# Performance work log

Measured on AMD Instinct MI355X. Metric: run time of the kernel, lower is better.

Reference implementation:

```python
import jax, jax.numpy as jnp
import numpy as np

N = 4096
FIN = 4096
LOC = 16
H1, H2, HEADS = 120, 50, 4
H1_PER = H1 // HEADS
FILM_Z = 32
SSDB_H = 60
N_HEMI = N // 2
NEG_SLOPE = 0.1
GATE_BIAS = -2.0
MASK_FILL = -9e15


def leaky(x):
    return jax.nn.leaky_relu(x, negative_slope=NEG_SLOPE)


def gat(x, mask, W, a_src, a_dst, bias, concat):
    # x: (N, Fin), W: (H, Fin, O), a_src/a_dst: (H, O), mask: (N, N) bool
    wh = jnp.einsum('nf,hfo->hno', x, W)            # (H, N, O)
    f1 = jnp.einsum('hno,ho->hn', wh, a_src)        # (H, N)
    f2 = jnp.einsum('hno,ho->hn', wh, a_dst)        # (H, N)
    e = leaky(f1[:, :, None] + f2[:, None, :])      # (H, N, N)
    e = jnp.where(mask[None], e, MASK_FILL)
    alpha = jax.nn.softmax(e, axis=-1)
    out = jnp.einsum('hij,hjo->hio', alpha, wh)     # (H, N, O)
    if concat:
        h, n, o = out.shape
        out2 = out.transpose(1, 0, 2).reshape(n, h * o)
    else:
        out2 = out.mean(axis=0)
    return out2 + bias


def _uni(k, shape, stdv):
    return jax.random.uniform(k, shape, jnp.float32, -stdv, stdv)


def setup_inputs() -> dict:
    key = jax.random.key(0)
    ks = jax.random.split(key, 30)
    s1 = 1.0 / np.sqrt(H1_PER)
    s2 = 1.0 / np.sqrt(H2)
    inp = {
        'x_fc': jax.random.normal(ks[0], (N, FIN), jnp.float32),
        'adj': jax.random.randint(ks[1], (N, N), 0, 2, jnp.int32),
        'l_loc': jax.random.uniform(ks[2], (N, LOC), jnp.float32),
        # gat1
        'W1': _uni(ks[3], (HEADS, FIN, H1_PER), s1),
        'a1s': _uni(ks[4], (HEADS, H1_PER), s1),
        'a1d': _uni(ks[5], (HEADS, H1_PER), s1),
        'b1': _uni(ks[6], (H1,), s1),
        # gat2
        'W2': _uni(ks[7], (1, H1, H2), s2),
        'a2s': _uni(ks[8], (1, H2), s2),
        'a2d': _uni(ks[9], (1, H2), s2),
        'b2': _uni(ks[10], (H2,), s2),
        # classifier (no bias)
        'Wc': _uni(ks[11], (2, H2), s2),
        # FiLM trunk
        'Wl1': _uni(ks[12], (FILM_Z, LOC), 1.0 / np.sqrt(LOC)),
        'bl1': _uni(ks[13], (FILM_Z,), 1.0 / np.sqrt(LOC)),
        'Wl2': _uni(ks[14], (FILM_Z, FILM_Z), 1.0 / np.sqrt(FILM_Z)),
        'bl2': _uni(ks[15], (FILM_Z,), 1.0 / np.sqrt(FILM_Z)),
        'Wg': _uni(ks[16], (H2, FILM_Z), 1.0 / np.sqrt(FILM_Z)),
        'bg': _uni(ks[17], (H2,), 1.0 / np.sqrt(FILM_Z)),
        'Wb': _uni(ks[18], (H2, FILM_Z), 1.0 / np.sqrt(FILM_Z)),
        'bb': _uni(ks[19], (H2,), 1.0 / np.sqrt(FILM_Z)),
        'Wgate': _uni(ks[20], (1, FILM_Z), 1.0 / np.sqrt(FILM_Z)),
        'bgate': jnp.full((1,), GATE_BIAS, jnp.float32),
        # SSDB hemi
        'Ws1': _uni(ks[21], (SSDB_H, N_HEMI), 1.0 / np.sqrt(N_HEMI)),
        'bs1': _uni(ks[22], (SSDB_H,), 1.0 / np.sqrt(N_HEMI)),
        'Ws2': _uni(ks[23], (1, SSDB_H), 1.0 / np.sqrt(SSDB_H)),
        'bs2': _uni(ks[24], (1,), 1.0 / np.sqrt(SSDB_H)),
    }
    return inp


def reference(x_fc, adj, l_loc, W1, a1s, a1d, b1, W2, a2s, a2d, b2, Wc,
              Wl1, bl1, Wl2, bl2, Wg, bg, Wb, bb, Wgate, bgate,
              Ws1, bs1, Ws2, bs2):
    mask = adj > 0
    h = leaky(gat(x_fc, mask, W1, a1s, a1d, b1, concat=True))    # (N, 120)
    h = leaky(gat(h, mask, W2, a2s, a2d, b2, concat=False))      # (N, 50)
    # FiLM conditioning
    z = leaky(l_loc @ Wl1.T + bl1)
    z = leaky(z @ Wl2.T + bl2)
    gamma = z @ Wg.T + bg                                        # (N, 50)
    beta = z @ Wb.T + bb                                         # (N, 50)
    g = jax.nn.sigmoid(z @ Wgate.T + bgate)                      # (N, 1)
    cov = jnp.clip(l_loc[:, -1], 0.0, 1.0)                       # coverage_power = 1.0
    g = g * cov[:, None]
    h_fused = h + g * (gamma * h + beta)
    logits = leaky(h_fused @ Wc.T)                               # (N, 2)
    # hemisphere SSDB bias
    t = logits.T                                                 # (2, N)
    ipsi = t[:, :N_HEMI]
    contra = t[:, N_HEMI:2 * N_HEMI]
    h_i = leaky(ipsi @ Ws1.T + bs1)                              # (2, 60)
    h_c = leaky(contra @ Ws1.T + bs1)
    b_i = leaky(h_i @ Ws2.T + bs2)                               # (2, 1)
    b_c = leaky(h_c @ Ws2.T + bs2)
    b_mid = 0.5 * (b_i + b_c)                                    # (2, 1)
    bias_nodes = jnp.concatenate([
        jnp.broadcast_to(b_i.T, (N_HEMI, 2)),
        jnp.broadcast_to(b_c.T, (N_HEMI, 2)),
    ], axis=0)                                                   # n_mid = 0
    logits = logits + bias_nodes
    bias_avg = b_mid[:, 0]                                       # (2,)
    return logits, bias_avg
```

## Files before the change

kernel.cpp:

```cpp
#include <hip/hip_runtime.h>

#define NN 4096
#define NNP 4128
#define BROW 132
#define HEADS 4
#define H1PER 30
#define H1DIM 120
#define H2DIM 50

typedef short short8_t __attribute__((ext_vector_type(8)));
typedef float f32x4 __attribute__((ext_vector_type(4)));

__device__ __forceinline__ float lrelu(float x) { return x > 0.f ? x : 0.1f * x; }

__device__ __forceinline__ unsigned short bfrne(float x) {
  unsigned u = __float_as_uint(x);
  u += 0x7fffu + ((u >> 16) & 1u);
  return (unsigned short)(u >> 16);
}
__device__ __forceinline__ unsigned bfpk_rne(float lo, float hi) {
  return (unsigned)bfrne(lo) | ((unsigned)bfrne(hi) << 16);
}
__device__ __forceinline__ unsigned bfpk(float lo, float hi) {
  unsigned a = (__float_as_uint(lo) + 0x8000u) >> 16;
  unsigned b = (__float_as_uint(hi) + 0x8000u) & 0xffff0000u;
  return a | b;
}
__device__ __forceinline__ unsigned fenc(float x) {
  unsigned u = __float_as_uint(x);
  return (u & 0x80000000u) ? ~u : (u | 0x80000000u);
}
__device__ __forceinline__ float fdec(unsigned u) {
  return (u & 0x80000000u) ? __uint_as_float(u ^ 0x80000000u) : __uint_as_float(~u);
}

__global__ __launch_bounds__(256) void k_bits(const int* __restrict__ adj,
                                              unsigned long long* __restrict__ bits) {
  int n = blockIdx.x >> 2, r = blockIdx.x & 3;
  size_t base = (size_t)n * 4096 + r * 1024;
  int t = threadIdx.x;
  int v0 = adj[base + t];
  int v1 = adj[base + 256 + t];
  int v2 = adj[base + 512 + t];
  int v3 = adj[base + 768 + t];
  unsigned long long m0 = __ballot(v0 > 0);
  unsigned long long m1 = __ballot(v1 > 0);
  unsigned long long m2 = __ballot(v2 > 0);
  unsigned long long m3 = __ballot(v3 > 0);
  if ((t & 63) == 0) {
    size_t w = (size_t)n * (BROW / 2) + r * 16 + (t >> 6);
    bits[w] = m0;
    bits[w + 4] = m1;
    bits[w + 8] = m2;
    bits[w + 12] = m3;
  }
}

__global__ __launch_bounds__(256) void k_prep(const float* __restrict__ W1,
                                              const float* __restrict__ a1s,
                                              const float* __restrict__ a1d,
                                              unsigned short* __restrict__ w1t) {
  int k = blockIdx.x * 256 + threadIdx.x;
#pragma unroll
  for (int h = 0; h < 4; ++h) {
    const float* wp = W1 + ((size_t)h * 4096 + k) * H1PER;
    float fs = 0.f, fd = 0.f;
#pragma unroll
    for (int oo = 0; oo < H1PER; ++oo) {
      float v = wp[oo];
      w1t[(size_t)(h * 30 + oo) * NNP + k] = bfrne(v);
      fs += v * a1s[h * H1PER + oo];
      fd += v * a1d[h * H1PER + oo];
    }
    w1t[(size_t)(120 + h) * NNP + k] = bfrne(fs);
    w1t[(size_t)(124 + h) * NNP + k] = bfrne(fd);
  }
}

__global__ __launch_bounds__(256) void k_gemm1s(const float* __restrict__ x,
                                                const unsigned short* __restrict__ w1t,
                                                float* __restrict__ part) {
  const int t = threadIdx.x;
  const int lane = t & 63, wave = t >> 6;
  const int m = lane & 15, q = lane >> 4;
  const int i0 = blockIdx.x * 32;
  const int kz = blockIdx.y * 512;
  const int r0 = (wave & 1) * 16;
  const int ntg0 = (wave >> 1) * 4;
  const float* xr = x + (size_t)(i0 + r0 + m) * 4096 + kz + q * 8;
  const unsigned short* wp = w1t + (size_t)m * NNP + kz + q * 8;
  f32x4 acc[4];
#pragma unroll
  for (int nt = 0; nt < 4; ++nt) acc[nt] = (f32x4){0.f, 0.f, 0.f, 0.f};
#pragma unroll
  for (int it = 0; it < 8; ++it) {
    const int kc = it * 64;
#pragma unroll
    for (int ks2 = 0; ks2 < 2; ++ks2) {
      const int ko = kc + ks2 * 32;
      float4 a0 = *(const float4*)(xr + ko);
      float4 a1 = *(const float4*)(xr + ko + 4);
      union { short8_t v; unsigned u[4]; } A;
      A.u[0] = bfpk_rne(a0.x, a0.y);
      A.u[1] = bfpk_rne(a0.z, a0.w);
      A.u[2] = bfpk_rne(a1.x, a1.y);
      A.u[3] = bfpk_rne(a1.z, a1.w);
      const unsigned short* wpp = wp + ko;
#pragma unroll
      for (int nt = 0; nt < 4; ++nt) {
        short8_t B = *(const short8_t*)(wpp + (size_t)(ntg0 + nt) * 16 * NNP);
        acc[nt] = __builtin_amdgcn_mfma_f32_16x16x32_bf16(A.v, B, acc[nt], 0, 0, 0);
      }
    }
  }
  float* pp = part + ((size_t)blockIdx.y * 4096 + i0 + r0 + q * 4) * 128 + ntg0 * 16 + m;
#pragma unroll
  for (int nt = 0; nt < 4; ++nt)
#pragma unroll
    for (int r = 0; r < 4; ++r) pp[r * 128 + nt * 16] = acc[nt][r];
}

__global__ __launch_bounds__(256) void k_f1c(const float* __restrict__ part,
                                             unsigned short* __restrict__ whbt,
                                             float* __restrict__ f1, float* __restrict__ f2,
                                             unsigned* __restrict__ mxu1) {
  const int t = threadIdx.x;
  const int n = blockIdx.x * 16 + (t >> 4);
  const int og = (t & 15) * 8;
  __shared__ float f2loc[16][4];
  float s[8] = {0.f, 0.f, 0.f, 0.f, 0.f, 0.f, 0.f, 0.f};
  for (int z = 0; z < 8; ++z) {
    const float* pp = part + ((size_t)z * NN + n) * 128 + og;
    float4 u0 = *(const float4*)pp;
    float4 u1 = *(const float4*)(pp + 4);
    s[0] += u0.x; s[1] += u0.y; s[2] += u0.z; s[3] += u0.w;
    s[4] += u1.x; s[5] += u1.y; s[6] += u1.z; s[7] += u1.w;
  }
  if (og < 120) {
#pragma unroll
    for (int j = 0; j < 8; ++j) {
      int o = og + j;
      int h = o / 30, oo = o - h * 30;
      whbt[(size_t)(h * 32 + oo) * NNP + n] = bfrne(s[j]);
    }
  } else {
#pragma unroll
    for (int j = 0; j < 4; ++j) {
      f1[(size_t)j * NN + n] = s[j];
      f2[(size_t)j * NN + n] = s[4 + j];
      f2loc[t >> 4][j] = s[4 + j];
    }
  }
  if ((t & 15) < 8) {
    int h = (t & 15) >> 1, odd = (t & 15) & 1;
    whbt[(size_t)(h * 32 + 30 + odd) * NNP + n] = odd ? 0 : 0x3f80;
  }
  __syncthreads();
  if (t < 4) {
    float m = f2loc[0][t];
#pragma unroll
    for (int i = 1; i < 16; ++i) m = fmaxf(m, f2loc[i][t]);
    atomicMax(&mxu1[t], fenc(m));
  }
}

__global__ __launch_bounds__(256) void k_att1m(const unsigned short* __restrict__ whbt,
                                               const float* __restrict__ f1, const float* __restrict__ f2,
                                               const unsigned* __restrict__ mxu1,
                                               const unsigned int* __restrict__ bits32,
                                               float* __restrict__ part) {
  const int h = blockIdx.y, js = blockIdx.z;
  const int t = threadIdx.x;
  const int lane = t & 63, wave = t >> 6;
  const int m = lane & 15, q = lane >> 4;
  const int i0 = blockIdx.x * 64 + wave * 16;
  const int jbase = js * 1024;
  const float mxh = fdec(mxu1[h]);
  __shared__ float2 es[1024];
  for (int e = t; e < 1024; e += 256) {
    float fv = f2[h * NN + jbase + e] - mxh;
    es[e] = make_float2(__expf(fv), __expf(0.1f * fv));
  }
  __syncthreads();
  const float f1r = f1[h * NN + i0 + m];
  const float s = f1r + mxh;
  const float R = __expf(fminf(60.f, -0.9f * s));
  const uint4* brow4 = (const uint4*)(bits32 + (size_t)(i0 + m) * BROW + (jbase >> 5));
  const unsigned short* bb0 = whbt + (size_t)(h * 32 + m) * NNP + jbase + q * 8;
  const unsigned short* bb1 = bb0 + 16 * NNP;
  const float2* fp = es + q * 8;
  f32x4 acc0 = {0.f, 0.f, 0.f, 0.f}, acc1 = {0.f, 0.f, 0.f, 0.f};
  for (int s4 = 0; s4 < 8; ++s4) {
    uint4 bq = brow4[s4];
#pragma unroll
    for (int sub = 0; sub < 4; ++sub) {
      const int step = s4 * 4 + sub;
      const int jl = step * 32;
      unsigned bsel = (sub == 0 ? bq.x : sub == 1 ? bq.y : sub == 2 ? bq.z : bq.w) >> (q * 8);
      float4 e01 = *(const float4*)(fp + jl);
      float4 e23 = *(const float4*)(fp + jl + 2);
      float4 e45 = *(const float4*)(fp + jl + 4);
      float4 e67 = *(const float4*)(fp + jl + 6);
      auto sc = [&](float ep, float en, int jj) {
        float wv = fmaxf(ep, R * en);
        return ((bsel >> jj) & 1u) ? wv : 0.f;
      };
      union { short8_t v; unsigned u[4]; } A;
      A.u[0] = bfpk(sc(e01.x, e01.y, 0), sc(e01.z, e01.w, 1));
      A.u[1] = bfpk(sc(e23.x, e23.y, 2), sc(e23.z, e23.w, 3));
      A.u[2] = bfpk(sc(e45.x, e45.y, 4), sc(e45.z, e45.w, 5));
      A.u[3] = bfpk(sc(e67.x, e67.y, 6), sc(e67.z, e67.w, 7));
      short8_t b0 = *(const short8_t*)(bb0 + jl);
      short8_t b1 = *(const short8_t*)(bb1 + jl);
      acc0 = __builtin_amdgcn_mfma_f32_16x16x32_bf16(A.v, b0, acc0, 0, 0, 0);
      acc1 = __builtin_amdgcn_mfma_f32_16x16x32_bf16(A.v, b1, acc1, 0, 0, 0);
    }
  }
  float* pp = part + ((size_t)(js * 4 + h) * NN + i0 + q * 4) * 32 + m;
#pragma unroll
  for (int r = 0; r < 4; ++r) {
    pp[r * 32] = acc0[r];
    pp[r * 32 + 16] = acc1[r];
  }
}

__global__ __launch_bounds__(256) void k_fuseA(const float* __restrict__ part, const float* __restrict__ b1,
                                               const float* __restrict__ W2, const float* __restrict__ a2s,
                                               const float* __restrict__ a2d,
                                               unsigned short* __restrict__ whbt2,
                                               float* __restrict__ f1b, float* __restrict__ f2b,
                                               unsigned* __restrict__ mxu2) {
  const int t = threadIdx.x;
  __shared__ float W2s[H1DIM * H2DIM];
  __shared__ float h1s[4][124];
  __shared__ float f2red[4];
  for (int e = t; e < H1DIM * H2DIM; e += 256) W2s[e] = W2[e];
  const int wv = t >> 6, lane = t & 63;
  const int n = blockIdx.x * 4 + wv;
  const int h = lane >> 4, o2 = (lane & 15) * 2;
  float tot0 = 0.f, tot1 = 0.f;
#pragma unroll
  for (int z = 0; z < 4; ++z) {
    const float* pp = part + ((size_t)(z * 4 + h) * NN + n) * 32 + o2;
    float2 u = *(const float2*)pp;
    tot0 += u.x;
    tot1 += u.y;
  }
  float l = __shfl(tot0, h * 16 + 15);
  float inv = 1.f / l;
  if (o2 < 30) {
    h1s[wv][h * 30 + o2] = lrelu(tot0 * inv + b1[h * 30 + o2]);
    h1s[wv][h * 30 + o2 + 1] = lrelu(tot1 * inv + b1[h * 30 + o2 + 1]);
  }
  __syncthreads();
  const int o = lane;
  float acc = 0.f;
  if (o < H2DIM) {
    const float* hr = h1s[wv];
#pragma unroll 4
    for (int k = 0; k < H1DIM; ++k) acc += hr[k] * W2s[k * H2DIM + o];
  }
  unsigned short wbv = (o < H2DIM) ? bfrne(acc) : (o == H2DIM ? (unsigned short)0x3f80 : (unsigned short)0);
  whbt2[(size_t)o * NNP + n] = wbv;
  float ps = (o < H2DIM) ? acc * a2s[o] : 0.f;
  float pd = (o < H2DIM) ? acc * a2d[o] : 0.f;
  for (int off = 32; off > 0; off >>= 1) {
    ps += __shfl_down(ps, off);
    pd += __shfl_down(pd, off);
  }
  if (lane == 0) {
    f1b[n] = ps;
    f2b[n] = pd;
    f2red[wv] = pd;
  }
  __syncthreads();
  if (t == 0) {
    float m = fmaxf(fmaxf(f2red[0], f2red[1]), fmaxf(f2red[2], f2red[3]));
    atomicMax(mxu2, fenc(m));
  }
}

__global__ __launch_bounds__(256) void k_att2m(const unsigned short* __restrict__ whbt2,
                                               const float* __restrict__ f1b, const float* __restrict__ f2b,
                                               const unsigned* __restrict__ mxu2,
                                               const unsigned int* __restrict__ bits32,
                                               float* __restrict__ part) {
  const int js = blockIdx.y;
  const int t = threadIdx.x;
  const int lane = t & 63, wave = t >> 6;
  const int m = lane & 15, q = lane >> 4;
  const int i0 = blockIdx.x * 64 + wave * 16;
  const int jbase = js * 512;
  const float mx0 = fdec(mxu2[0]);
  __shared__ float2 es[512];
  for (int e = t; e < 512; e += 256) {
    float fv = f2b[jbase + e] - mx0;
    es[e] = make_float2(__expf(fv), __expf(0.1f * fv));
  }
  __syncthreads();
  const float f1r = f1b[i0 + m];
  const float s = f1r + mx0;
  const float R = __expf(fminf(60.f, -0.9f * s));
  const uint4* brow4 = (const uint4*)(bits32 + (size_t)(i0 + m) * BROW + (jbase >> 5));
  const unsigned short* bb = whbt2 + (size_t)m * NNP + jbase + q * 8;
  const float2* fp = es + q * 8;
  f32x4 acc[4];
#pragma unroll
  for (int x = 0; x < 4; ++x) acc[x] = (f32x4){0.f, 0.f, 0.f, 0.f};
  for (int s4 = 0; s4 < 4; ++s4) {
    uint4 bq = brow4[s4];
#pragma unroll
    for (int sub = 0; sub < 4; ++sub) {
      const int step = s4 * 4 + sub;
      const int jl = step * 32;
      unsigned bsel = (sub == 0 ? bq.x : sub == 1 ? bq.y : sub == 2 ? bq.z : bq.w) >> (q * 8);
      float4 e01 = *(const float4*)(fp + jl);
      float4 e23 = *(const float4*)(fp + jl + 2);
      float4 e45 = *(const float4*)(fp + jl + 4);
      float4 e67 = *(const float4*)(fp + jl + 6);
      auto sc = [&](float ep, float en, int jj) {
        float wv = fmaxf(ep, R * en);
        return ((bsel >> jj) & 1u) ? wv : 0.f;
      };
      union { short8_t v; unsigned u[4]; } A;
      A.u[0] = bfpk(sc(e01.x, e01.y, 0), sc(e01.z, e01.w, 1));
      A.u[1] = bfpk(sc(e23.x, e23.y, 2), sc(e23.z, e23.w, 3));
      A.u[2] = bfpk(sc(e45.x, e45.y, 4), sc(e45.z, e45.w, 5));
      A.u[3] = bfpk(sc(e67.x, e67.y, 6), sc(e67.z, e67.w, 7));
#pragma unroll
      for (int tile = 0; tile < 4; ++tile) {
        short8_t b = *(const short8_t*)(bb + (size_t)tile * 16 * NNP + jl);
        acc[tile] = __builtin_amdgcn_mfma_f32_16x16x32_bf16(A.v, b, acc[tile], 0, 0, 0);
      }
    }
  }
  float* pp = part + ((size_t)js * NN + i0 + q * 4) * 64 + m;
#pragma unroll
  for (int tile = 0; tile < 4; ++tile)
#pragma unroll
    for (int r = 0; r < 4; ++r) pp[r * 64 + tile * 16] = acc[tile][r];
}

__global__ __launch_bounds__(256) void k_fuseB(const float* __restrict__ part, const float* __restrict__ b2,
                                               const float* __restrict__ l_loc,
                                               const float* __restrict__ Wl1, const float* __restrict__ bl1,
                                               const float* __restrict__ Wl2, const float* __restrict__ bl2,
                                               const float* __restrict__ Wg, const float* __restrict__ bg,
                                               const float* __restrict__ Wb, const float* __restrict__ bb,
                                               const float* __restrict__ Wgate, const float* __restrict__ bgate,
                                               const float* __restrict__ Wc, float* __restrict__ logits) {
  const int t = threadIdx.x;
  const int wv = t >> 6, lane = t & 63;
  const int n = blockIdx.x * 4 + wv;
  const float* p = part + (size_t)n * 64 + lane;
  float tot = 0.f;
#pragma unroll
  for (int z = 0; z < 8; ++z) tot += p[(size_t)z * NN * 64];
  float l = __shfl(tot, 50);
  float hv = (lane < H2DIM) ? lrelu(tot / l + b2[lane]) : 0.f;
  int r32 = lane & 31;
  float locv = l_loc[n * 16 + (lane & 15)];
  float cov = __shfl(locv, 15);
  cov = fminf(fmaxf(cov, 0.f), 1.f);
  float a1v = bl1[r32];
#pragma unroll
  for (int j = 0; j < 16; ++j) a1v += Wl1[r32 * 16 + j] * __shfl(locv, j);
  float z1 = lrelu(a1v);
  float a2v = bl2[r32];
#pragma unroll
  for (int j = 0; j < 32; ++j) a2v += Wl2[r32 * 32 + j] * __shfl(z1, j);
  float z2 = lrelu(a2v);
  float gs = bgate[0];
  float gam, bet;
  {
    int o = lane < H2DIM ? lane : 0;
    gam = bg[o];
    bet = bb[o];
#pragma unroll
    for (int j = 0; j < 32; ++j) {
      float zj = __shfl(z2, j);
      gs += Wgate[j] * zj;
      gam += Wg[o * 32 + j] * zj;
      bet += Wb[o * 32 + j] * zj;
    }
  }
  float g = cov / (1.f + __expf(-gs));
  float hf = hv + g * (gam * hv + bet);
  int o = lane < H2DIM ? lane : 0;
  float p0 = lane < H2DIM ? hf * Wc[o] : 0.f;
  float p1 = lane < H2DIM ? hf * Wc[H2DIM + o] : 0.f;
  for (int off = 32; off > 0; off >>= 1) {
    p0 += __shfl_down(p0, off);
    p1 += __shfl_down(p1, off);
  }
  if (lane == 0) {
    logits[n * 2 + 0] = lrelu(p0);
    logits[n * 2 + 1] = lrelu(p1);
  }
}

__global__ __launch_bounds__(64) void k_ssdbA(const float* __restrict__ logits,
                                              const float* __restrict__ Ws1, const float* __restrict__ bs1,
                                              const float* __restrict__ Ws2, float* __restrict__ hsum) {
  const int k = blockIdx.x, combo = blockIdx.y;
  const int hemi = combo >> 1, c = combo & 1;
  const int lane = threadIdx.x;
  const float* wr = Ws1 + (size_t)k * 2048;
  const float* lc = logits + (size_t)hemi * 4096 + c;
  float acc = 0.f;
#pragma unroll 4
  for (int i = lane; i < 2048; i += 64) acc += wr[i] * lc[2 * i];
  for (int off = 32; off > 0; off >>= 1) acc += __shfl_down(acc, off);
  if (lane == 0) hsum[combo * 60 + k] = lrelu(acc + bs1[k]) * Ws2[k];
}

__global__ __launch_bounds__(256) void k_finB(const float* __restrict__ hsum,
                                              const float* __restrict__ bs2,
                                              const float* __restrict__ logits,
                                              float* __restrict__ out) {
  __shared__ float Bs[4];
  const int t = threadIdx.x;
  {
    int combo = t >> 6, k = t & 63;
    float v = (k < 60) ? hsum[combo * 60 + k] : 0.f;
    for (int off = 32; off > 0; off >>= 1) v += __shfl_down(v, off);
    if (k == 0) Bs[combo] = lrelu(v + bs2[0]);
  }
  __syncthreads();
  int id = blockIdx.x * 256 + t;
  if (id < 2 * NN) {
    int n = id >> 1, c = id & 1;
    out[id] = logits[id] + Bs[(n < 2048 ? 0 : 2) + c];
  } else if (id < 2 * NN + 2) {
    int c = id - 2 * NN;
    out[id] = 0.5f * (Bs[c] + Bs[2 + c]);
  }
}

#define OFF_BITS 0
#define OFF_W1T 540672
#define OFF_GP 804864
#define OFF_A1P 804864
#define OFF_A2P 804864
#define OFF_WH1BT 4999168
#define OFF_F1A 5263360
#define OFF_F2A 5279744
#define OFF_WH2BT 5296128
#define OFF_F12 5428224
#define OFF_F22 5432320
#define OFF_LOG 5436416
#define OFF_MX 5444608
#define OFF_HS 5444672

extern "C" void kernel_launch(void* const* d_in, const int* in_sizes, int n_in,
                              void* d_out, int out_size, void* d_ws, size_t ws_size,
                              hipStream_t stream) {
  const float* x_fc  = (const float*)d_in[0];
  const int*   adj   = (const int*)d_in[1];
  const float* l_loc = (const float*)d_in[2];
  const float* W1    = (const float*)d_in[3];
  const float* a1s   = (const float*)d_in[4];
  const float* a1d   = (const float*)d_in[5];
  const float* b1    = (const float*)d_in[6];
  const float* W2    = (const float*)d_in[7];
  const float* a2s   = (const float*)d_in[8];
  const float* a2d   = (const float*)d_in[9];
  const float* b2    = (const float*)d_in[10];
  const float* Wc    = (const float*)d_in[11];
  const float* Wl1   = (const float*)d_in[12];
  const float* bl1   = (const float*)d_in[13];
  const float* Wl2   = (const float*)d_in[14];
  const float* bl2   = (const float*)d_in[15];
  const float* Wg    = (const float*)d_in[16];
  const float* bg    = (const float*)d_in[17];
  const float* Wb    = (const float*)d_in[18];
  const float* bb    = (const float*)d_in[19];
  const float* Wgate = (const float*)d_in[20];
  const float* bgate = (const float*)d_in[21];
  const float* Ws1   = (const float*)d_in[22];
  const float* bs1   = (const float*)d_in[23];
  const float* Ws2   = (const float*)d_in[24];
  const float* bs2   = (const float*)d_in[25];
  float* out = (float*)d_out;
  float* w = (float*)d_ws;
  unsigned long long* bits = (unsigned long long*)(w + OFF_BITS);
  const unsigned int* bits32 = (const unsigned int*)bits;
  unsigned short* wh1bt = (unsigned short*)(w + OFF_WH1BT);
  unsigned short* wh2bt = (unsigned short*)(w + OFF_WH2BT);
  unsigned short* w1t = (unsigned short*)(w + OFF_W1T);
  unsigned* mxu = (unsigned*)(w + OFF_MX);

  hipMemsetAsync(mxu, 0, 8 * sizeof(unsigned), stream);
  k_bits<<<NN * NN / 1024, 256, 0, stream>>>(adj, bits);
  k_prep<<<16, 256, 0, stream>>>(W1, a1s, a1d, w1t);
  k_gemm1s<<<dim3(128, 8), 256, 0, stream>>>(x_fc, w1t, w + OFF_GP);
  k_f1c<<<256, 256, 0, stream>>>(w + OFF_GP, wh1bt, w + OFF_F1A, w + OFF_F2A, mxu);
  k_att1m<<<dim3(64, HEADS, 4), 256, 0, stream>>>(wh1bt, w + OFF_F1A, w + OFF_F2A,
                                                  mxu, bits32, w + OFF_A1P);
  k_fuseA<<<1024, 256, 0, stream>>>(w + OFF_A1P, b1, W2, a2s, a2d, wh2bt,
                                    w + OFF_F12, w + OFF_F22, mxu + 4);
  k_att2m<<<dim3(64, 8), 256, 0, stream>>>(wh2bt, w + OFF_F12, w + OFF_F22,
                                           mxu + 4, bits32, w + OFF_A2P);
  k_fuseB<<<1024, 256, 0, stream>>>(w + OFF_A2P, b2, l_loc, Wl1, bl1, Wl2, bl2,
                                    Wg, bg, Wb, bb, Wgate, bgate, Wc, w + OFF_LOG);
  k_ssdbA<<<dim3(60, 4), 64, 0, stream>>>(w + OFF_LOG, Ws1, bs1, Ws2, w + OFF_HS);
  k_finB<<<33, 256, 0, stream>>>(w + OFF_HS, bs2, w + OFF_LOG, out);
}
```

Baseline: 335.8 us.

## Stage gemm1 operands through LDS with async global_load_lds double buffering

The first GAT projection GEMM now loads its x and W1 tiles into per-wave LDS buffers using the direct global-to-LDS load instruction. The buffers are double-buffered so the next k-slice streams in while MFMAs run on the current one, with XOR swizzles to avoid bank conflicts. This targets exposed global-load latency in the unpipelined register-load loop. In exchange it uses 48KB of LDS per block, which may reduce occupancy, and it relies on hand-written vmcnt waits.

```diff
diff --git a/kernel.cpp b/kernel.cpp
--- a/kernel.cpp
+++ b/kernel.cpp
@@ -33,6 +33,10 @@
 __device__ __forceinline__ float fdec(unsigned u) {
   return (u & 0x80000000u) ? __uint_as_float(u ^ 0x80000000u) : __uint_as_float(~u);
 }
+
+#define GL16(g, l)                                                                        \
+  __builtin_amdgcn_global_load_lds((const __attribute__((address_space(1))) unsigned int*)(g), \
+                                   (__attribute__((address_space(3))) unsigned int*)(l), 16, 0, 0)
 
 __global__ __launch_bounds__(256) void k_bits(const int* __restrict__ adj,
                                               unsigned long long* __restrict__ bits) {
@@ -87,30 +91,53 @@
   const int kz = blockIdx.y * 512;
   const int r0 = (wave & 1) * 16;
   const int ntg0 = (wave >> 1) * 4;
-  const float* xr = x + (size_t)(i0 + r0 + m) * 4096 + kz + q * 8;
-  const unsigned short* wp = w1t + (size_t)m * NNP + kz + q * 8;
+  __shared__ __align__(16) unsigned char lds[4][2][6144];
+  unsigned char* my0 = &lds[wave][0][0];
+  unsigned char* my1 = &lds[wave][1][0];
+  const int arow = lane >> 3;
+  const int agc = (lane & 7) ^ (arow & 7);
+  const int bgc = (lane & 3) ^ ((lane >> 3) & 3);
+  const float* gxa0 = x + (size_t)(i0 + r0 + arow) * 4096 + kz + agc * 4;
+  const float* gxa1 = gxa0 + (size_t)8 * 4096;
+  const unsigned short* gwb = w1t + (size_t)(ntg0 * 16 + (lane >> 2)) * NNP + kz + bgc * 8;
+  const int as0 = ((2 * q) ^ (m & 7)) * 16;
+  const int as1 = ((2 * q + 1) ^ (m & 7)) * 16;
+  const int bso = m * 64 + (q ^ ((m >> 1) & 3)) * 16;
+  const int abase = m * 128;
   f32x4 acc[4];
 #pragma unroll
   for (int nt = 0; nt < 4; ++nt) acc[nt] = (f32x4){0.f, 0.f, 0.f, 0.f};
-#pragma unroll
-  for (int it = 0; it < 8; ++it) {
-    const int kc = it * 64;
-#pragma unroll
-    for (int ks2 = 0; ks2 < 2; ++ks2) {
-      const int ko = kc + ks2 * 32;
-      float4 a0 = *(const float4*)(xr + ko);
-      float4 a1 = *(const float4*)(xr + ko + 4);
-      union { short8_t v; unsigned u[4]; } A;
-      A.u[0] = bfpk_rne(a0.x, a0.y);
-      A.u[1] = bfpk_rne(a0.z, a0.w);
-      A.u[2] = bfpk_rne(a1.x, a1.y);
-      A.u[3] = bfpk_rne(a1.z, a1.w);
-      const unsigned short* wpp = wp + ko;
-#pragma unroll
-      for (int nt = 0; nt < 4; ++nt) {
-        short8_t B = *(const short8_t*)(wpp + (size_t)(ntg0 + nt) * 16 * NNP);
-        acc[nt] = __builtin_amdgcn_mfma_f32_16x16x32_bf16(A.v, B, acc[nt], 0, 0, 0);
-      }
+
+  auto STAGE = [&](unsigned char* d, int kk) {
+    GL16(gxa0 + kk, d + lane * 16);
+    GL16(gxa1 + kk, d + 1024 + lane * 16);
+#pragma unroll
+    for (int c = 0; c < 4; ++c)
+      GL16(gwb + (size_t)c * 16 * NNP + kk, d + 2048 + c * 1024 + lane * 16);
+  };
+
+  STAGE(my0, 0);
+#pragma unroll
+  for (int it = 0; it < 16; ++it) {
+    unsigned char* cur = (it & 1) ? my1 : my0;
+    if (it < 15) {
+      STAGE((it & 1) ? my0 : my1, (it + 1) * 32);
+      asm volatile("s_waitcnt vmcnt(6)" ::: "memory");
+    } else {
+      asm volatile("s_waitcnt vmcnt(0)" ::: "memory");
+    }
+    __builtin_amdgcn_sched_barrier(0);
+    float4 a0 = *(const float4*)(cur + abase + as0);
+    float4 a1 = *(const float4*)(cur + abase + as1);
+    union { short8_t v; unsigned u[4]; } A;
+    A.u[0] = bfpk_rne(a0.x, a0.y);
+    A.u[1] = bfpk_rne(a0.z, a0.w);
+    A.u[2] = bfpk_rne(a1.x, a1.y);
+    A.u[3] = bfpk_rne(a1.z, a1.w);
+#pragma unroll
+    for (int nt = 0; nt < 4; ++nt) {
+      short8_t B = *(const short8_t*)(cur + 2048 + nt * 1024 + bso);
+      acc[nt] = __builtin_amdgcn_mfma_f32_16x16x32_bf16(A.v, B, acc[nt], 0, 0, 0);
     }
   }
   float* pp = part + ((size_t)blockIdx.y * 4096 + i0 + r0 + q * 4) * 128 + ntg0 * 16 + m;
```

After: 333.0 us. No clear change (-0.8%).

## Stage GEMM1 tiles into LDS with async double-buffered loads and 16-way split-K

Applied to the files above, without the earlier changes.

The first-layer projection GEMM now copies x and weight tiles into shared memory with global_load_lds, double-buffered and XOR-swizzled, so loads for the next step overlap the MFMAs on the current one. Before, each wave read operands straight from global memory with no reuse. The K split doubles from 8 to 16, which gives more blocks, and the reduction kernel and workspace offsets grow to match. The cost is a larger partial-sum buffer to write and reduce, plus barriers on every iteration.

```diff
diff --git a/kernel.cpp b/kernel.cpp
--- a/kernel.cpp
+++ b/kernel.cpp
@@ -33,6 +33,10 @@
 __device__ __forceinline__ float fdec(unsigned u) {
   return (u & 0x80000000u) ? __uint_as_float(u ^ 0x80000000u) : __uint_as_float(~u);
 }
+
+#define GL16(g, l)                                                                        \
+  __builtin_amdgcn_global_load_lds((const __attribute__((address_space(1))) unsigned int*)(g), \
+                                   (__attribute__((address_space(3))) unsigned int*)(l), 16, 0, 0)
 
 __global__ __launch_bounds__(256) void k_bits(const int* __restrict__ adj,
                                               unsigned long long* __restrict__ bits) {
@@ -84,34 +88,63 @@
   const int lane = t & 63, wave = t >> 6;
   const int m = lane & 15, q = lane >> 4;
   const int i0 = blockIdx.x * 32;
-  const int kz = blockIdx.y * 512;
+  const int kz = blockIdx.y * 256;
+  __shared__ float xs[2][32 * 32];
+  __shared__ unsigned short bsm[2][128 * 32];
   const int r0 = (wave & 1) * 16;
   const int ntg0 = (wave >> 1) * 4;
-  const float* xr = x + (size_t)(i0 + r0 + m) * 4096 + kz + q * 8;
-  const unsigned short* wp = w1t + (size_t)m * NNP + kz + q * 8;
+  const int ar = t >> 3;
+  const float* gxa = x + (size_t)(i0 + ar) * 4096 + kz + ((t & 7) ^ (ar & 7)) * 4;
+  const int adst = ar * 32 + (t & 7) * 4;
+  const int rB0 = t >> 2;
+  const int rB1 = 64 + (t >> 2);
+  const int gc0 = (t & 3) ^ (rB0 & 3) ^ ((rB0 >> 2) & 3);
+  const int gc1 = (t & 3) ^ (rB1 & 3) ^ ((rB1 >> 2) & 3);
+  const unsigned short* gwb0 = w1t + (size_t)rB0 * NNP + kz + gc0 * 8;
+  const unsigned short* gwb1 = w1t + (size_t)rB1 * NNP + kz + gc1 * 8;
+  const int bdst0 = rB0 * 32 + (t & 3) * 8;
+  const int bdst1 = rB1 * 32 + (t & 3) * 8;
+  const int arow = r0 + m;
+  const int as0 = ((2 * q) ^ (arow & 7)) * 4;
+  const int as1 = (((2 * q) + 1) ^ (arow & 7)) * 4;
   f32x4 acc[4];
 #pragma unroll
   for (int nt = 0; nt < 4; ++nt) acc[nt] = (f32x4){0.f, 0.f, 0.f, 0.f};
+
+  auto STAGE = [&](int buf, int kk) {
+    GL16(gxa + kk, &xs[buf][adst]);
+    GL16(gwb0 + kk, &bsm[buf][bdst0]);
+    GL16(gwb1 + kk, &bsm[buf][bdst1]);
+  };
+
+  STAGE(0, 0);
 #pragma unroll
   for (int it = 0; it < 8; ++it) {
-    const int kc = it * 64;
-#pragma unroll
-    for (int ks2 = 0; ks2 < 2; ++ks2) {
-      const int ko = kc + ks2 * 32;
-      float4 a0 = *(const float4*)(xr + ko);
-      float4 a1 = *(const float4*)(xr + ko + 4);
-      union { short8_t v; unsigned u[4]; } A;
-      A.u[0] = bfpk_rne(a0.x, a0.y);
-      A.u[1] = bfpk_rne(a0.z, a0.w);
-      A.u[2] = bfpk_rne(a1.x, a1.y);
-      A.u[3] = bfpk_rne(a1.z, a1.w);
-      const unsigned short* wpp = wp + ko;
-#pragma unroll
-      for (int nt = 0; nt < 4; ++nt) {
-        short8_t B = *(const short8_t*)(wpp + (size_t)(ntg0 + nt) * 16 * NNP);
-        acc[nt] = __builtin_amdgcn_mfma_f32_16x16x32_bf16(A.v, B, acc[nt], 0, 0, 0);
-      }
-    }
+    const int cur = it & 1;
+    if (it < 7) {
+      STAGE(cur ^ 1, (it + 1) * 32);
+      asm volatile("s_waitcnt vmcnt(3)" ::: "memory");
+    } else {
+      asm volatile("s_waitcnt vmcnt(0)" ::: "memory");
+    }
+    __builtin_amdgcn_s_barrier();
+    __builtin_amdgcn_sched_barrier(0);
+    float4 a0 = *(const float4*)&xs[cur][arow * 32 + as0];
+    float4 a1 = *(const float4*)&xs[cur][arow * 32 + as1];
+    union { short8_t v; unsigned u[4]; } A;
+    A.u[0] = bfpk_rne(a0.x, a0.y);
+    A.u[1] = bfpk_rne(a0.z, a0.w);
+    A.u[2] = bfpk_rne(a1.x, a1.y);
+    A.u[3] = bfpk_rne(a1.z, a1.w);
+#pragma unroll
+    for (int nt = 0; nt < 4; ++nt) {
+      const int rb = (ntg0 + nt) * 16 + m;
+      const int cb = q ^ (rb & 3) ^ ((rb >> 2) & 3);
+      short8_t B = *(const short8_t*)&bsm[cur][rb * 32 + cb * 8];
+      acc[nt] = __builtin_amdgcn_mfma_f32_16x16x32_bf16(A.v, B, acc[nt], 0, 0, 0);
+    }
+    __builtin_amdgcn_sched_barrier(0);
+    __builtin_amdgcn_s_barrier();
   }
   float* pp = part + ((size_t)blockIdx.y * 4096 + i0 + r0 + q * 4) * 128 + ntg0 * 16 + m;
 #pragma unroll
@@ -129,7 +162,7 @@
   const int og = (t & 15) * 8;
   __shared__ float f2loc[16][4];
   float s[8] = {0.f, 0.f, 0.f, 0.f, 0.f, 0.f, 0.f, 0.f};
-  for (int z = 0; z < 8; ++z) {
+  for (int z = 0; z < 16; ++z) {
     const float* pp = part + ((size_t)z * NN + n) * 128 + og;
     float4 u0 = *(const float4*)pp;
     float4 u1 = *(const float4*)(pp + 4);
@@ -442,15 +475,15 @@
 #define OFF_GP 804864
 #define OFF_A1P 804864
 #define OFF_A2P 804864
-#define OFF_WH1BT 4999168
-#define OFF_F1A 5263360
-#define OFF_F2A 5279744
-#define OFF_WH2BT 5296128
-#define OFF_F12 5428224
-#define OFF_F22 5432320
-#define OFF_LOG 5436416
-#define OFF_MX 5444608
-#define OFF_HS 5444672
+#define OFF_WH1BT 9193472
+#define OFF_F1A 9457664
+#define OFF_F2A 9474048
+#define OFF_WH2BT 9490432
+#define OFF_F12 9622528
+#define OFF_F22 9626624
+#define OFF_LOG 9630720
+#define OFF_MX 9638912
+#define OFF_HS 9638976
 
 extern "C" void kernel_launch(void* const* d_in, const int* in_sizes, int n_in,
                               void* d_out, int out_size, void* d_ws, size_t ws_size,
@@ -493,7 +526,7 @@
   hipMemsetAsync(mxu, 0, 8 * sizeof(unsigned), stream);
   k_bits<<<NN * NN / 1024, 256, 0, stream>>>(adj, bits);
   k_prep<<<16, 256, 0, stream>>>(W1, a1s, a1d, w1t);
-  k_gemm1s<<<dim3(128, 8), 256, 0, stream>>>(x_fc, w1t, w + OFF_GP);
+  k_gemm1s<<<dim3(128, 16), 256, 0, stream>>>(x_fc, w1t, w + OFF_GP);
   k_f1c<<<256, 256, 0, stream>>>(w + OFF_GP, wh1bt, w + OFF_F1A, w + OFF_F2A, mxu);
   k_att1m<<<dim3(64, HEADS, 4), 256, 0, stream>>>(wh1bt, w + OFF_F1A, w + OFF_F2A,
                                                   mxu, bits32, w + OFF_A1P);
```

New measurement: 319.9 us. 4.7% less time.
